# Optimization experiments

Hardware: AMD Instinct MI355X
Metric: run time of the kernel (lower is better)

Reference implementation:

```python
import jax, jax.numpy as jnp
import numpy as np

V, E, H, OUT = 32000, 256, 256, 32000
B, TE, TD = 16, 128, 64


def gru_layer(x, h0, Wih, Whh, bih, bhh, lengths):
    """PyTorch-semantics GRU over padded batch-first x:(B,T,I), h0:(B,H).
    Emulates pack/pad: hidden frozen and output zeroed past each sample's length."""
    T = x.shape[1]

    def step(h, inp):
        xt, t = inp  # xt:(B,I)
        gi = xt @ Wih.T + bih          # (B,3H)
        gh = h @ Whh.T + bhh
        ir, iz, inn = jnp.split(gi, 3, axis=-1)
        hr, hz, hn = jnp.split(gh, 3, axis=-1)
        r = jax.nn.sigmoid(ir + hr)
        z = jax.nn.sigmoid(iz + hz)
        n = jnp.tanh(inn + r * hn)
        hnew = (1.0 - z) * n + z * h
        valid = (t < lengths)[:, None]
        h = jnp.where(valid, hnew, h)
        out = jnp.where(valid, hnew, 0.0)
        return h, out

    hT, ys = jax.lax.scan(step, h0, (jnp.swapaxes(x, 0, 1), jnp.arange(T)))
    return jnp.swapaxes(ys, 0, 1), hT  # (B,T,H), (B,H)


def setup_inputs() -> dict:
    key = jax.random.key(0)
    ks = jax.random.split(key, 20)
    s = 0.05
    enc_len = jax.random.randint(ks[0], (B,), 1, TE + 1).at[0].set(TE)
    dec_len = jax.random.randint(ks[1], (B,), 1, TD + 1).at[0].set(TD)
    return {
        "encoder_input": jax.random.randint(ks[2], (B, TE), 0, V),
        "encoder_length": enc_len,
        "decoder_input": jax.random.randint(ks[3], (B, TD), 0, V),
        "decoder_length": dec_len,
        "embedding": jax.random.normal(ks[4], (V, E)) * s,
        "enc_Wih": jax.random.normal(ks[5], (3 * H, E)) * s,
        "enc_Whh": jax.random.normal(ks[6], (3 * H, H)) * s,
        "enc_bih": jax.random.normal(ks[7], (3 * H,)) * s,
        "enc_bhh": jax.random.normal(ks[8], (3 * H,)) * s,
        "dec_Wih": jax.random.normal(ks[9], (3 * H, E)) * s,
        "dec_Whh": jax.random.normal(ks[10], (3 * H, H)) * s,
        "dec_bih": jax.random.normal(ks[11], (3 * H,)) * s,
        "dec_bhh": jax.random.normal(ks[12], (3 * H,)) * s,
        "attn_W": jax.random.normal(ks[13], (H, 2 * H)) * s,
        "attn_Wb": jnp.zeros((H,)),
        "attn_v": jax.random.normal(ks[14], (1, H)) * s,
        "attn_vb": jnp.zeros((1,)),
        "dense_W": jax.random.normal(ks[15], (H, 2 * H)) * s,
        "dense_b": jnp.zeros((H,)),
        "out_W": jax.random.normal(ks[16], (OUT, H)) * s,
        "out_b": jnp.zeros((OUT,)),
    }


def reference(encoder_input, encoder_length, decoder_input, decoder_length,
              embedding, enc_Wih, enc_Whh, enc_bih, enc_bhh,
              dec_Wih, dec_Whh, dec_bih, dec_bhh,
              attn_W, attn_Wb, attn_v, attn_vb,
              dense_W, dense_b, out_W, out_b):
    enc_x = embedding[encoder_input]  # (B,TE,E)
    dec_x = embedding[decoder_input]  # (B,TD,E)

    h0 = jnp.zeros((B, H), dtype=enc_x.dtype)
    enc_out, enc_h = gru_layer(enc_x, h0, enc_Wih, enc_Whh, enc_bih, enc_bhh, encoder_length)
    dec_out, _ = gru_layer(dec_x, enc_h, dec_Wih, dec_Whh, dec_bih, dec_bhh, decoder_length)

    # --- additive attention with per-sample length mask ---
    enc_valid = jnp.arange(TE) < encoder_length[:, None]     # (B,TE)
    dec_valid = jnp.arange(TD) < decoder_length[:, None]     # (B,TD)
    mask = (dec_valid[:, :, None] & enc_valid[:, None, :]).astype(enc_out.dtype)[..., None]  # (B,TD,TE,1)

    enc_e = enc_out[:, None, :, :] * mask  # (B,TD,TE,H)
    dec_e = dec_out[:, :, None, :] * mask  # (B,TD,TE,H)

    score = jnp.tanh(jnp.concatenate([enc_e, dec_e], axis=3) @ attn_W.T + attn_Wb)
    energy = score @ attn_v.T + attn_vb  # (B,TD,TE,1)
    a = jax.nn.softmax(energy, axis=2)   # softmax over encoder steps (unmasked, as original)
    aw = a * mask
    s = aw.sum(axis=2)                   # (B,TD,1)
    s = jnp.where(s == 0, 1.0, s)
    attention = aw / s[:, :, None, :]
    context = (attention * enc_e).sum(axis=2)  # (B,TD,H); dropout is identity (eval)

    outputs = jnp.concatenate([dec_out, context], axis=2)  # (B,TD,2H)
    dense = jnp.tanh(outputs @ dense_W.T + dense_b)
    logits = dense @ out_W.T + out_b  # (B,TD,OUT)
    return logits
```

## Files before the change

### kernel.cpp

```cpp
#include <hip/hip_runtime.h>
#include <hip/hip_bf16.h>

typedef unsigned short ushort_t;
typedef unsigned int uint_t;
typedef unsigned long long u64_t;

#define BB 16
#define TE 128
#define TD 64
#define HH 256
#define G3 768
#define KK 256
#define OUTV 32000
#define MROWS_E (BB*TE)
#define MROWS_D (BB*TD)
#define NBLK 16
#define JD 16
#define QW_PER_BUF 2048

typedef __attribute__((ext_vector_type(8))) short short8;
typedef __attribute__((ext_vector_type(4))) float f32x4;

__device__ __forceinline__ float b2f(ushort_t u) {
  union { uint_t i; float f; } v; v.i = ((uint_t)u) << 16; return v.f;
}
__device__ __forceinline__ ushort_t f2b(float f) {
  union { float f; uint_t i; } v; v.f = f;
  uint_t x = v.i;
  return (ushort_t)((x + 0x7fffu + ((x >> 16) & 1u)) >> 16);
}
__device__ __forceinline__ float ldf(const void* p, size_t i, uint_t f32f) {
  return f32f ? ((const float*)p)[i] : b2f(((const ushort_t*)p)[i]);
}
__device__ __forceinline__ float fsig(float x) { return 1.f/(1.f + __expf(-x)); }
__device__ __forceinline__ float ftanh(float x) { return 1.f - 2.f/(__expf(2.f*x) + 1.f); }

__global__ __launch_bounds__(256) void detect_kernel(const void* emb, uint_t* flag) {
  int tid = threadIdx.x;
  uint_t w = ((const uint_t*)emb)[tid];
  uint_t e = (w >> 7) & 0xFFu;
  bool pass = (e >= 100u && e <= 127u);
  unsigned long long m = __ballot(pass);
  __shared__ int cnt[4];
  if ((tid & 63) == 0) cnt[tid >> 6] = __popcll(m);
  __syncthreads();
  if (tid == 0) {
    int c = cnt[0] + cnt[1] + cnt[2] + cnt[3];
    *flag = (c >= 128) ? 0u : 1u;
  }
}

__global__ __launch_bounds__(256) void prep_kernel(
    const void* eWhh, const void* dWhh, const void* denseW, const void* outW,
    const void* ebih, const void* ebhh, const void* dbih, const void* dbhh,
    const void* outb, const uint_t* flagp,
    ushort_t* WBe, ushort_t* WBd, ushort_t* DWT, ushort_t* obW,
    float* cbe, float* cbd, float* obf, u64_t* hq) {
  uint_t f = *flagp;
  int tid = blockIdx.x * blockDim.x + threadIdx.x;
  int nth = gridDim.x * blockDim.x;
  for (int i = tid; i < G3*KK; i += nth) {
    WBe[i] = f2b(ldf(eWhh, i, f));
    WBd[i] = f2b(ldf(dWhh, i, f));
  }
  for (int i = tid; i < 512*HH; i += nth) {
    int k = i / HH, c = i % HH;
    DWT[i] = f2b(ldf(denseW, (size_t)c*512 + k, f));
  }
  for (size_t i = tid; i < (size_t)OUTV*HH; i += nth) obW[i] = f2b(ldf(outW, i, f));
  for (int i = tid; i < G3; i += nth) {
    float be = ldf(ebih, i, f), bd = ldf(dbih, i, f);
    if (i < 2*HH) { be += ldf(ebhh, i, f); bd += ldf(dbhh, i, f); }
    cbe[i] = be; cbd[i] = bd;
  }
  for (int i = tid; i < OUTV; i += nth) obf[i] = ldf(outb, i, f);
  for (int i = tid; i < 2*QW_PER_BUF; i += nth) hq[i] = 0ull;
}

#define LDT 264

__global__ __launch_bounds__(256) void gemm_kernel(
    const ushort_t* A, const int* tokens, const void* emb,
    const void* Bw, int ldb, int b_off,
    const float* bias, const uint_t* flagp,
    float* Cf, ushort_t* Cb, int ldc, int M, int tshift, int a_f32, int b_bf16) {
  __shared__ __align__(16) ushort_t Bs[64*LDT];
  __shared__ __align__(16) ushort_t As[32*LDT];
  uint_t f = *flagp;
  int tid = threadIdx.x;
  int wave = tid >> 6, lane = tid & 63;
  int n0 = blockIdx.x * 64;
#pragma unroll
  for (int it = 0; it < 8; ++it) {
    int idx = it*256 + tid;
    int row = idx >> 5, col = (idx & 31) << 3;
    size_t e = (size_t)(n0 + row)*ldb + col + b_off;
    uint4 v;
    if (f && !b_bf16) {
      const float4* s = (const float4*)((const float*)Bw + e);
      float4 x = s[0], y = s[1];
      v.x = (uint_t)f2b(x.x) | ((uint_t)f2b(x.y) << 16);
      v.y = (uint_t)f2b(x.z) | ((uint_t)f2b(x.w) << 16);
      v.z = (uint_t)f2b(y.x) | ((uint_t)f2b(y.y) << 16);
      v.w = (uint_t)f2b(y.z) | ((uint_t)f2b(y.w) << 16);
    } else {
      v = *(const uint4*)((const ushort_t*)Bw + e);
    }
    *(uint4*)(Bs + row*LDT + col) = v;
  }
  int arow_i = lane & 15;
  float bias_v = 0.f;
  if (bias) bias_v = bias[n0 + wave*16 + arow_i];
  int koff = (lane >> 4) << 3;
  for (int m0 = blockIdx.y*32; m0 < M; m0 += gridDim.y*32) {
    __syncthreads();
#pragma unroll
    for (int it = 0; it < 4; ++it) {
      int idx = it*256 + tid;
      int row = idx >> 5, col = (idx & 31) << 3;
      uint4 v;
      if (tokens) {
        size_t e = (size_t)tokens[m0 + row]*KK + col;
        if (f) {
          const float4* s = (const float4*)((const float*)emb + e);
          float4 x = s[0], y = s[1];
          v.x = (uint_t)f2b(x.x) | ((uint_t)f2b(x.y) << 16);
          v.y = (uint_t)f2b(x.z) | ((uint_t)f2b(x.w) << 16);
          v.z = (uint_t)f2b(y.x) | ((uint_t)f2b(y.y) << 16);
          v.w = (uint_t)f2b(y.z) | ((uint_t)f2b(y.w) << 16);
        } else {
          v = *(const uint4*)((const ushort_t*)emb + e);
        }
      } else if (a_f32) {
        const float4* s = (const float4*)((const float*)A + (size_t)(m0 + row)*KK + col);
        float4 x = s[0], y = s[1];
        v.x = (uint_t)f2b(x.x) | ((uint_t)f2b(x.y) << 16);
        v.y = (uint_t)f2b(x.z) | ((uint_t)f2b(x.w) << 16);
        v.z = (uint_t)f2b(y.x) | ((uint_t)f2b(y.y) << 16);
        v.w = (uint_t)f2b(y.z) | ((uint_t)f2b(y.w) << 16);
      } else {
        v = *(const uint4*)(A + (size_t)(m0 + row)*KK + col);
      }
      *(uint4*)(As + row*LDT + col) = v;
    }
    __syncthreads();
#pragma unroll
    for (int msub = 0; msub < 2; ++msub) {
      f32x4 acc = {0.f,0.f,0.f,0.f};
      const ushort_t* ap = As + (msub*16 + arow_i)*LDT + koff;
      const ushort_t* bp = Bs + (wave*16 + arow_i)*LDT + koff;
#pragma unroll
      for (int ks = 0; ks < 8; ++ks) {
        short8 af = *(const short8*)(ap + ks*32);
        short8 bf = *(const short8*)(bp + ks*32);
        acc = __builtin_amdgcn_mfma_f32_16x16x32_bf16(af, bf, acc, 0, 0, 0);
      }
      int mbase = m0 + msub*16 + (lane >> 4)*4;
      int ncol = n0 + wave*16 + arow_i;
#pragma unroll
      for (int r = 0; r < 4; ++r) {
        float val = acc[r] + bias_v;
        int mr = mbase + r;
        int orow = tshift ? (((mr & ((1 << tshift) - 1)) << 4) + (mr >> tshift)) : mr;
        if (Cf) Cf[(size_t)orow*ldc + ncol] = val;
        else    Cb[(size_t)orow*ldc + ncol] = f2b(val);
      }
    }
  }
}

#define HSBF 264

__device__ __forceinline__ void stage_w(const ushort_t* WB, int j0, int tid,
                                        ushort_t* wlds) {
#pragma unroll
  for (int it = 0; it < 6; ++it) {
    int idx = it*256 + tid;
    int row = idx >> 5, col = (idx & 31) << 3;
    const ushort_t* src = WB + ((size_t)((row >> 4)*HH + j0 + (row & 15)))*KK + col;
    *(uint4*)(wlds + row*HSBF + col) = *(const uint4*)src;
  }
}

__global__ __launch_bounds__(256) void gru_kernel(
    const float* gi_e, const float* gi_d, const ushort_t* WBe, const ushort_t* WBd,
    const void* ebhh, const void* dbhh, const uint_t* flagp,
    const int* elen, const int* dlen, float* eout, float* dout, u64_t* hq) {
  uint_t f = *flagp;
  __shared__ __align__(16) ushort_t wlds[48*HSBF];
  __shared__ __align__(16) float part[2][4][3][16][17];
  const int tid = threadIdx.x;
  const int wave = tid >> 6, lane = tid & 63;
  const int mrow = lane & 15, quad = lane >> 4;
  const int j0 = blockIdx.x * JD;
  const int m = tid >> 4, n = tid & 15;
  const int j = j0 + n;
  const int je = j & ~1;
  const int widx = ((je >> 6) << 9) + (((je >> 5) & 1) << 8)
                 + (((je >> 1) & 3) << 6) + (((je >> 3) & 3) << 4) + m;

  stage_w(WBe, j0, tid, wlds);
  const float bn_e = ldf(ebhh, 2*HH + j, f);
  const float bn_d = ldf(dbhh, 2*HH + j, f);
  const int len_e = elen[m], len_d = dlen[m];
  float hreg = 0.f;
  float grv = gi_e[(size_t)m*G3 + j];
  float gzv = gi_e[(size_t)m*G3 + HH + j];
  float gnv = gi_e[(size_t)m*G3 + 2*HH + j];
  __syncthreads();

  for (int s = 0; s < TE + TD; ++s) {
    if (s == TE) {
      stage_w(WBd, j0, tid, wlds);
      __syncthreads();
    }
    const bool enc = s < TE;
    const int t = enc ? s : s - TE;
    const u64_t* hbR = hq + (size_t)(s & 1)*QW_PER_BUF + wave*512 + lane;
    u64_t qv[8];
    const uint_t target = (uint_t)s;
    int guard = 0;
    for (;;) {
      bool ok = true;
#pragma unroll
      for (int ks = 0; ks < 2; ++ks)
#pragma unroll
        for (int i = 0; i < 4; ++i) {
          qv[ks*4 + i] = __hip_atomic_load(hbR + ks*256 + i*64,
                                           __ATOMIC_RELAXED, __HIP_MEMORY_SCOPE_AGENT);
          ok = ok && ((uint_t)qv[ks*4 + i] == target);
        }
      if (__all(ok) || ++guard > 30000) break;
    }
    f32x4 ar = {0.f,0.f,0.f,0.f}, az = {0.f,0.f,0.f,0.f}, an = {0.f,0.f,0.f,0.f};
#pragma unroll
    for (int ks = 0; ks < 2; ++ks) {
      union { uint_t u[4]; short8 s8; } av;
#pragma unroll
      for (int i = 0; i < 4; ++i) av.u[i] = (uint_t)(qv[ks*4 + i] >> 32);
      const ushort_t* wp = wlds + mrow*HSBF + wave*64 + ks*32 + quad*8;
      short8 b0 = *(const short8*)(wp);
      short8 b1 = *(const short8*)(wp + 16*HSBF);
      short8 b2 = *(const short8*)(wp + 32*HSBF);
      ar = __builtin_amdgcn_mfma_f32_16x16x32_bf16(av.s8, b0, ar, 0, 0, 0);
      az = __builtin_amdgcn_mfma_f32_16x16x32_bf16(av.s8, b1, az, 0, 0, 0);
      an = __builtin_amdgcn_mfma_f32_16x16x32_bf16(av.s8, b2, an, 0, 0, 0);
    }
    const int p = s & 1;
#pragma unroll
    for (int r = 0; r < 4; ++r) {
      part[p][wave][0][quad*4 + r][mrow] = ar[r];
      part[p][wave][1][quad*4 + r][mrow] = az[r];
      part[p][wave][2][quad*4 + r][mrow] = an[r];
    }
    __syncthreads();
    float accr = 0.f, accz = 0.f, accn = 0.f;
#pragma unroll
    for (int w = 0; w < 4; ++w) {
      accr += part[p][w][0][m][n];
      accz += part[p][w][1][m][n];
      accn += part[p][w][2][m][n];
    }
    float rr = fsig(grv + accr);
    float zz = fsig(gzv + accz);
    float nn = ftanh(gnv + rr*(accn + (enc ? bn_e : bn_d)));
    float hc = (1.f - zz)*nn + zz*hreg;
    bool valid = t < (enc ? len_e : len_d);
    float ov = valid ? hc : 0.f;
    hreg = valid ? hc : hreg;
    if (enc) eout[((size_t)(m*TE + t))*HH + j] = ov;
    else     dout[((size_t)(m*TD + t))*HH + j] = ov;
    uint_t h16 = (uint_t)f2b(hreg);
    uint_t up = (uint_t)__shfl_down((int)h16, 1);
    if (!(n & 1)) {
      u64_t q = ((u64_t)(h16 | (up << 16)) << 32) | (u64_t)(uint_t)(s + 1);
      __hip_atomic_store(hq + (size_t)((s + 1) & 1)*QW_PER_BUF + widx,
                         q, __ATOMIC_RELAXED, __HIP_MEMORY_SCOPE_AGENT);
    }
    int s2 = s + 1;
    if (s2 < TE + TD) {
      const float* g2 = (s2 < TE) ? (gi_e + (size_t)(s2*BB + m)*G3)
                                  : (gi_d + (size_t)((s2 - TE)*BB + m)*G3);
      grv = g2[j]; gzv = g2[HH + j]; gnv = g2[2*HH + j];
    }
  }
}

__global__ __launch_bounds__(256) void attn_kernel(
    const float* eprj, const float* dprj, const float* eout, const float* dout,
    const void* Wb, const void* av, const void* avb,
    const ushort_t* DWT, const void* db, const uint_t* flagp,
    const int* elen, const int* dlen, ushort_t* dense_bf) {
  int bd = blockIdx.x;
  int b = bd / TD, td = bd % TD;
  int tid = threadIdx.x;
  int wave = tid >> 6, lane = tid & 63;
  uint_t f = *flagp;
  __shared__ float dp[HH], dsrow[HH], vv[HH], att[TE];
  int el = elen[b];
  bool dok = td < dlen[b];
  size_t drow = (size_t)bd * HH;
  dp[tid] = dprj[drow + tid] + ldf(Wb, tid, f);
  dsrow[tid] = dout[drow + tid];
  vv[tid] = ldf(av, tid, f);
  if (tid < TE) att[tid] = 0.f;
  __syncthreads();
  float ctx = 0.f;
  if (dok) {
    float vb0 = ldf(avb, 0, f);
    int nteb = (el + 3) >> 2;
    for (int teb = 0; teb < nteb; ++teb) {
      int te = teb*4 + wave;
      if (te < el) {
        const float* ep = eprj + (size_t)(b*TE + te)*HH;
        float s = 0.f;
#pragma unroll
        for (int i = 0; i < 4; ++i) {
          int hh = lane + 64*i;
          s += ftanh(ep[hh] + dp[hh]) * vv[hh];
        }
#pragma unroll
        for (int off = 32; off > 0; off >>= 1) s += __shfl_xor(s, off);
        if (lane == 0) att[te] = s + vb0;
      }
    }
    __syncthreads();
    float mx = -1e30f;
    for (int te = 0; te < el; ++te) mx = fmaxf(mx, att[te]);
    __syncthreads();
    if (tid < el) att[tid] = __expf(att[tid] - mx);
    __syncthreads();
    float ssum = 0.f;
    for (int te = 0; te < el; ++te) ssum += att[te];
    float inv = (ssum > 0.f) ? 1.f/ssum : 0.f;
    const float* ebase = eout + (size_t)(b*TE)*HH + tid;
    float c0 = 0.f, c1 = 0.f, c2 = 0.f, c3 = 0.f;
    int te = 0;
    for (; te + 4 <= el; te += 4) {
      c0 += att[te    ] * ebase[(size_t)(te    )*HH];
      c1 += att[te + 1] * ebase[(size_t)(te + 1)*HH];
      c2 += att[te + 2] * ebase[(size_t)(te + 2)*HH];
      c3 += att[te + 3] * ebase[(size_t)(te + 3)*HH];
    }
    for (; te < el; ++te) c0 += att[te] * ebase[(size_t)te*HH];
    ctx = (c0 + c1 + c2 + c3) * inv;
  }
  __syncthreads();
  dp[tid] = ctx;
  __syncthreads();
  const ushort_t* w0 = DWT + tid;
  float a0 = ldf(db, tid, f), a1 = 0.f, a2 = 0.f, a3 = 0.f;
#pragma unroll 8
  for (int k = 0; k < HH; k += 4) {
    a0 = fmaf(b2f(w0[(size_t)(k    )*HH]), dsrow[k    ], a0);
    a1 = fmaf(b2f(w0[(size_t)(k + 1)*HH]), dsrow[k + 1], a1);
    a2 = fmaf(b2f(w0[(size_t)(k + 2)*HH]), dsrow[k + 2], a2);
    a3 = fmaf(b2f(w0[(size_t)(k + 3)*HH]), dsrow[k + 3], a3);
  }
#pragma unroll 8
  for (int k = 0; k < HH; k += 4) {
    a0 = fmaf(b2f(w0[(size_t)(HH + k    )*HH]), dp[k    ], a0);
    a1 = fmaf(b2f(w0[(size_t)(HH + k + 1)*HH]), dp[k + 1], a1);
    a2 = fmaf(b2f(w0[(size_t)(HH + k + 2)*HH]), dp[k + 2], a2);
    a3 = fmaf(b2f(w0[(size_t)(HH + k + 3)*HH]), dp[k + 3], a3);
  }
  dense_bf[drow + tid] = f2b(ftanh(a0 + a1 + a2 + a3));
}

extern "C" void kernel_launch(void* const* d_in, const int* in_sizes, int n_in,
                              void* d_out, int out_size, void* d_ws, size_t ws_size,
                              hipStream_t stream) {
  const int* enc_in   = (const int*)d_in[0];
  const int* enc_len  = (const int*)d_in[1];
  const int* dec_in   = (const int*)d_in[2];
  const int* dec_len  = (const int*)d_in[3];
  const void* emb    = d_in[4];
  const void* eWih   = d_in[5];
  const void* eWhh   = d_in[6];
  const void* ebih   = d_in[7];
  const void* ebhh   = d_in[8];
  const void* dWih   = d_in[9];
  const void* dWhh   = d_in[10];
  const void* dbih   = d_in[11];
  const void* dbhh   = d_in[12];
  const void* attnW  = d_in[13];
  const void* attnWb = d_in[14];
  const void* attnv  = d_in[15];
  const void* attnvb = d_in[16];
  const void* denseW = d_in[17];
  const void* denseb = d_in[18];
  const void* outW   = d_in[19];
  const void* outb   = d_in[20];
  float* out = (float*)d_out;

  float* ws = (float*)d_ws;
  size_t o = 0;
  uint_t* flag = (uint_t*)(ws + o);   o += 4;
  u64_t* hq = (u64_t*)(ws + o);       o += 4*QW_PER_BUF;
  ushort_t* WBe = (ushort_t*)(ws + o); o += G3*KK/2;
  ushort_t* WBd = (ushort_t*)(ws + o); o += G3*KK/2;
  ushort_t* DWT = (ushort_t*)(ws + o); o += 512*HH/2;
  ushort_t* obW = (ushort_t*)(ws + o); o += (size_t)OUTV*HH/2;
  float* cbe = ws + o;                o += G3;
  float* cbd = ws + o;                o += G3;
  float* obf = ws + o;                o += OUTV;
  float* gi_e = ws + o;               o += (size_t)MROWS_E*G3;
  float* gi_d = ws + o;               o += (size_t)MROWS_D*G3;
  float* eout = ws + o;               o += (size_t)MROWS_E*HH;
  float* dout = ws + o;               o += (size_t)MROWS_D*HH;
  float* eprj = ws + o;               o += (size_t)MROWS_E*HH;
  float* dprj = ws + o;               o += (size_t)MROWS_D*HH;
  ushort_t* dense_bf = (ushort_t*)(ws + o); o += (size_t)MROWS_D*HH/2;

  detect_kernel<<<1, 256, 0, stream>>>(emb, flag);
  prep_kernel<<<384, 256, 0, stream>>>(eWhh, dWhh, denseW, outW, ebih, ebhh, dbih,
                                       dbhh, outb, flag, WBe, WBd, DWT, obW,
                                       cbe, cbd, obf, hq);
  gemm_kernel<<<dim3(12,8), 256, 0, stream>>>(nullptr, enc_in, emb, eWih, 256, 0,
                                              cbe, flag, gi_e, nullptr, G3, MROWS_E, 7, 0, 0);
  gemm_kernel<<<dim3(12,4), 256, 0, stream>>>(nullptr, dec_in, emb, dWih, 256, 0,
                                              cbd, flag, gi_d, nullptr, G3, MROWS_D, 6, 0, 0);
  gru_kernel<<<NBLK, 256, 0, stream>>>(gi_e, gi_d, WBe, WBd, ebhh, dbhh, flag,
                                       enc_len, dec_len, eout, dout, hq);
  gemm_kernel<<<dim3(4,16), 256, 0, stream>>>((const ushort_t*)eout, nullptr, nullptr,
                                              attnW, 512, 0, nullptr, flag, eprj,
                                              nullptr, HH, MROWS_E, 0, 1, 0);
  gemm_kernel<<<dim3(4,8), 256, 0, stream>>>((const ushort_t*)dout, nullptr, nullptr,
                                             attnW, 512, 256, nullptr, flag, dprj,
                                             nullptr, HH, MROWS_D, 0, 1, 0);
  attn_kernel<<<MROWS_D, 256, 0, stream>>>(eprj, dprj, eout, dout, attnWb, attnv, attnvb,
                                           DWT, denseb, flag, enc_len, dec_len, dense_bf);
  gemm_kernel<<<dim3(500,4), 256, 0, stream>>>(dense_bf, nullptr, nullptr, obW, 256, 0,
                                               obf, flag, out, nullptr, OUTV, MROWS_D, 0, 0, 1);
}
```

Baseline: 786.4 us.

## Use single-wave GRU blocks, fuse dtype detection into prep, vectorize outW conversion

The recurrent GRU kernel now runs one 64-lane wave per block, which does the full K=256 reduction with 8 MFMA steps. This removes the per-step LDS partial-sum exchange and __syncthreads, shortening the latency-bound serial chain of 192 steps. The cost is 4x more polled atomic loads per lane and longer MFMA chains in a single wave. Separately, the dtype-detect kernel is merged into prep_kernel, saving a launch, and the 32000x256 output weight conversion now moves 8 elements per iteration with vector loads and stores.

After: 936.8 us. 19.1% more time.

```diff
diff --git a/kernel.cpp b/kernel.cpp
--- a/kernel.cpp
+++ b/kernel.cpp
@@ -35,39 +35,48 @@
 __device__ __forceinline__ float fsig(float x) { return 1.f/(1.f + __expf(-x)); }
 __device__ __forceinline__ float ftanh(float x) { return 1.f - 2.f/(__expf(2.f*x) + 1.f); }
 
-__global__ __launch_bounds__(256) void detect_kernel(const void* emb, uint_t* flag) {
-  int tid = threadIdx.x;
-  uint_t w = ((const uint_t*)emb)[tid];
+__global__ __launch_bounds__(256) void prep_kernel(
+    const void* emb, const void* eWhh, const void* dWhh, const void* denseW,
+    const void* outW, const void* ebih, const void* ebhh, const void* dbih,
+    const void* dbhh, const void* outb, uint_t* flag,
+    ushort_t* WBe, ushort_t* WBd, ushort_t* DWT, ushort_t* obW,
+    float* cbe, float* cbd, float* obf, u64_t* hq) {
+  int ltid = threadIdx.x;
+  uint_t w = ((const uint_t*)emb)[ltid];
   uint_t e = (w >> 7) & 0xFFu;
   bool pass = (e >= 100u && e <= 127u);
-  unsigned long long m = __ballot(pass);
+  unsigned long long mb = __ballot(pass);
   __shared__ int cnt[4];
-  if ((tid & 63) == 0) cnt[tid >> 6] = __popcll(m);
+  if ((ltid & 63) == 0) cnt[ltid >> 6] = __popcll(mb);
   __syncthreads();
-  if (tid == 0) {
-    int c = cnt[0] + cnt[1] + cnt[2] + cnt[3];
-    *flag = (c >= 128) ? 0u : 1u;
-  }
-}
-
-__global__ __launch_bounds__(256) void prep_kernel(
-    const void* eWhh, const void* dWhh, const void* denseW, const void* outW,
-    const void* ebih, const void* ebhh, const void* dbih, const void* dbhh,
-    const void* outb, const uint_t* flagp,
-    ushort_t* WBe, ushort_t* WBd, ushort_t* DWT, ushort_t* obW,
-    float* cbe, float* cbd, float* obf, u64_t* hq) {
-  uint_t f = *flagp;
-  int tid = blockIdx.x * blockDim.x + threadIdx.x;
+  int c = cnt[0] + cnt[1] + cnt[2] + cnt[3];
+  uint_t f = (c >= 128) ? 0u : 1u;
+  if (blockIdx.x == 0 && ltid == 0) *flag = f;
+  int tid = blockIdx.x * blockDim.x + ltid;
   int nth = gridDim.x * blockDim.x;
   for (int i = tid; i < G3*KK; i += nth) {
     WBe[i] = f2b(ldf(eWhh, i, f));
     WBd[i] = f2b(ldf(dWhh, i, f));
   }
   for (int i = tid; i < 512*HH; i += nth) {
-    int k = i / HH, c = i % HH;
-    DWT[i] = f2b(ldf(denseW, (size_t)c*512 + k, f));
-  }
-  for (size_t i = tid; i < (size_t)OUTV*HH; i += nth) obW[i] = f2b(ldf(outW, i, f));
+    int k = i / HH, cc = i % HH;
+    DWT[i] = f2b(ldf(denseW, (size_t)cc*512 + k, f));
+  }
+  const int OW8 = OUTV*HH/8;
+  for (int i = tid; i < OW8; i += nth) {
+    uint4 v;
+    if (f) {
+      const float4* s = (const float4*)outW + (size_t)i*2;
+      float4 x = s[0], y = s[1];
+      v.x = (uint_t)f2b(x.x) | ((uint_t)f2b(x.y) << 16);
+      v.y = (uint_t)f2b(x.z) | ((uint_t)f2b(x.w) << 16);
+      v.z = (uint_t)f2b(y.x) | ((uint_t)f2b(y.y) << 16);
+      v.w = (uint_t)f2b(y.z) | ((uint_t)f2b(y.w) << 16);
+    } else {
+      v = ((const uint4*)outW)[i];
+    }
+    ((uint4*)obW)[i] = v;
+  }
   for (int i = tid; i < G3; i += nth) {
     float be = ldf(ebih, i, f), bd = ldf(dbih, i, f);
     if (i < 2*HH) { be += ldf(ebhh, i, f); bd += ldf(dbhh, i, f); }
@@ -171,74 +180,75 @@
 
 #define HSBF 264
 
-__device__ __forceinline__ void stage_w(const ushort_t* WB, int j0, int tid,
-                                        ushort_t* wlds) {
-#pragma unroll
-  for (int it = 0; it < 6; ++it) {
-    int idx = it*256 + tid;
+__device__ __forceinline__ void stage_w64(const ushort_t* WB, int j0, int lane,
+                                          ushort_t* wlds) {
+#pragma unroll
+  for (int it = 0; it < 24; ++it) {
+    int idx = it*64 + lane;
     int row = idx >> 5, col = (idx & 31) << 3;
     const ushort_t* src = WB + ((size_t)((row >> 4)*HH + j0 + (row & 15)))*KK + col;
     *(uint4*)(wlds + row*HSBF + col) = *(const uint4*)src;
   }
 }
 
-__global__ __launch_bounds__(256) void gru_kernel(
+__global__ __launch_bounds__(64, 1) void gru_kernel(
     const float* gi_e, const float* gi_d, const ushort_t* WBe, const ushort_t* WBd,
     const void* ebhh, const void* dbhh, const uint_t* flagp,
     const int* elen, const int* dlen, float* eout, float* dout, u64_t* hq) {
   uint_t f = *flagp;
   __shared__ __align__(16) ushort_t wlds[48*HSBF];
-  __shared__ __align__(16) float part[2][4][3][16][17];
-  const int tid = threadIdx.x;
-  const int wave = tid >> 6, lane = tid & 63;
-  const int mrow = lane & 15, quad = lane >> 4;
-  const int j0 = blockIdx.x * JD;
-  const int m = tid >> 4, n = tid & 15;
-  const int j = j0 + n;
-  const int je = j & ~1;
-  const int widx = ((je >> 6) << 9) + (((je >> 5) & 1) << 8)
-                 + (((je >> 1) & 3) << 6) + (((je >> 3) & 3) << 4) + m;
-
-  stage_w(WBe, j0, tid, wlds);
+  const int lane = threadIdx.x;
+  const int l15 = lane & 15, quad = lane >> 4;
+  const int wreg = blockIdx.x;
+  const int j0 = wreg * JD;
+  const int j = j0 + l15;
+
+  stage_w64(WBe, j0, lane, wlds);
   const float bn_e = ldf(ebhh, 2*HH + j, f);
   const float bn_d = ldf(dbhh, 2*HH + j, f);
-  const int len_e = elen[m], len_d = dlen[m];
-  float hreg = 0.f;
-  float grv = gi_e[(size_t)m*G3 + j];
-  float gzv = gi_e[(size_t)m*G3 + HH + j];
-  float gnv = gi_e[(size_t)m*G3 + 2*HH + j];
-  __syncthreads();
+  int lene_r[4], lend_r[4];
+#pragma unroll
+  for (int r = 0; r < 4; ++r) {
+    lene_r[r] = elen[quad*4 + r];
+    lend_r[r] = dlen[quad*4 + r];
+  }
+  float hreg[4] = {0.f, 0.f, 0.f, 0.f};
+  float gr[4], gz[4], gn[4];
+#pragma unroll
+  for (int r = 0; r < 4; ++r) {
+    const float* gp = gi_e + (size_t)(quad*4 + r)*G3;
+    gr[r] = gp[j]; gz[r] = gp[HH + j]; gn[r] = gp[2*HH + j];
+  }
+  const int pubbase = wreg*128 + (l15 >> 1)*16 + quad*4;
+  const bool dopub = !(l15 & 1);
 
   for (int s = 0; s < TE + TD; ++s) {
-    if (s == TE) {
-      stage_w(WBd, j0, tid, wlds);
-      __syncthreads();
-    }
+    if (s == TE) stage_w64(WBd, j0, lane, wlds);
     const bool enc = s < TE;
     const int t = enc ? s : s - TE;
-    const u64_t* hbR = hq + (size_t)(s & 1)*QW_PER_BUF + wave*512 + lane;
-    u64_t qv[8];
+    const u64_t* hbR = hq + (size_t)(s & 1)*QW_PER_BUF + quad*64 + l15;
+    u64_t qv[32];
     const uint_t target = (uint_t)s;
     int guard = 0;
     for (;;) {
       bool ok = true;
 #pragma unroll
-      for (int ks = 0; ks < 2; ++ks)
-#pragma unroll
-        for (int i = 0; i < 4; ++i) {
-          qv[ks*4 + i] = __hip_atomic_load(hbR + ks*256 + i*64,
+      for (int ks = 0; ks < 8; ++ks)
+#pragma unroll
+        for (int e = 0; e < 4; ++e) {
+          qv[ks*4 + e] = __hip_atomic_load(hbR + ks*256 + e*16,
                                            __ATOMIC_RELAXED, __HIP_MEMORY_SCOPE_AGENT);
-          ok = ok && ((uint_t)qv[ks*4 + i] == target);
+          ok = ok && ((uint_t)qv[ks*4 + e] == target);
         }
       if (__all(ok) || ++guard > 30000) break;
     }
     f32x4 ar = {0.f,0.f,0.f,0.f}, az = {0.f,0.f,0.f,0.f}, an = {0.f,0.f,0.f,0.f};
 #pragma unroll
-    for (int ks = 0; ks < 2; ++ks) {
+    for (int ks = 0; ks < 8; ++ks) {
       union { uint_t u[4]; short8 s8; } av;
 #pragma unroll
-      for (int i = 0; i < 4; ++i) av.u[i] = (uint_t)(qv[ks*4 + i] >> 32);
-      const ushort_t* wp = wlds + mrow*HSBF + wave*64 + ks*32 + quad*8;
+      for (int e = 0; e < 4; ++e) av.u[e] = (uint_t)(qv[ks*4 + e] >> 32);
+      const ushort_t* wp = wlds + l15*HSBF + ks*32 + quad*8;
       short8 b0 = *(const short8*)(wp);
       short8 b1 = *(const short8*)(wp + 16*HSBF);
       short8 b2 = *(const short8*)(wp + 32*HSBF);
@@ -246,42 +256,43 @@
       az = __builtin_amdgcn_mfma_f32_16x16x32_bf16(av.s8, b1, az, 0, 0, 0);
       an = __builtin_amdgcn_mfma_f32_16x16x32_bf16(av.s8, b2, an, 0, 0, 0);
     }
-    const int p = s & 1;
+    const float bn = enc ? bn_e : bn_d;
 #pragma unroll
     for (int r = 0; r < 4; ++r) {
-      part[p][wave][0][quad*4 + r][mrow] = ar[r];
-      part[p][wave][1][quad*4 + r][mrow] = az[r];
-      part[p][wave][2][quad*4 + r][mrow] = an[r];
-    }
-    __syncthreads();
-    float accr = 0.f, accz = 0.f, accn = 0.f;
-#pragma unroll
-    for (int w = 0; w < 4; ++w) {
-      accr += part[p][w][0][m][n];
-      accz += part[p][w][1][m][n];
-      accn += part[p][w][2][m][n];
-    }
-    float rr = fsig(grv + accr);
-    float zz = fsig(gzv + accz);
-    float nn = ftanh(gnv + rr*(accn + (enc ? bn_e : bn_d)));
-    float hc = (1.f - zz)*nn + zz*hreg;
-    bool valid = t < (enc ? len_e : len_d);
-    float ov = valid ? hc : 0.f;
-    hreg = valid ? hc : hreg;
-    if (enc) eout[((size_t)(m*TE + t))*HH + j] = ov;
-    else     dout[((size_t)(m*TD + t))*HH + j] = ov;
-    uint_t h16 = (uint_t)f2b(hreg);
-    uint_t up = (uint_t)__shfl_down((int)h16, 1);
-    if (!(n & 1)) {
-      u64_t q = ((u64_t)(h16 | (up << 16)) << 32) | (u64_t)(uint_t)(s + 1);
-      __hip_atomic_store(hq + (size_t)((s + 1) & 1)*QW_PER_BUF + widx,
-                         q, __ATOMIC_RELAXED, __HIP_MEMORY_SCOPE_AGENT);
+      float rr = fsig(gr[r] + ar[r]);
+      float zz = fsig(gz[r] + az[r]);
+      float nn = ftanh(gn[r] + rr*(an[r] + bn));
+      float hc = (1.f - zz)*nn + zz*hreg[r];
+      bool valid = t < (enc ? lene_r[r] : lend_r[r]);
+      float ov = valid ? hc : 0.f;
+      hreg[r] = valid ? hc : hreg[r];
+      int m = quad*4 + r;
+      if (enc) eout[((size_t)(m*TE + t))*HH + j] = ov;
+      else     dout[((size_t)(m*TD + t))*HH + j] = ov;
+    }
+    uint_t h16[4], up[4];
+#pragma unroll
+    for (int r = 0; r < 4; ++r) {
+      h16[r] = (uint_t)f2b(hreg[r]);
+      up[r] = (uint_t)__shfl_down((int)h16[r], 1);
+    }
+    if (dopub) {
+      u64_t* hbW = hq + (size_t)((s + 1) & 1)*QW_PER_BUF + pubbase;
+#pragma unroll
+      for (int r = 0; r < 4; ++r) {
+        u64_t q = ((u64_t)(h16[r] | (up[r] << 16)) << 32) | (u64_t)(uint_t)(s + 1);
+        __hip_atomic_store(hbW + r, q, __ATOMIC_RELAXED, __HIP_MEMORY_SCOPE_AGENT);
+      }
     }
     int s2 = s + 1;
     if (s2 < TE + TD) {
-      const float* g2 = (s2 < TE) ? (gi_e + (size_t)(s2*BB + m)*G3)
-                                  : (gi_d + (size_t)((s2 - TE)*BB + m)*G3);
-      grv = g2[j]; gzv = g2[HH + j]; gnv = g2[2*HH + j];
+      const float* gbase = (s2 < TE) ? gi_e + (size_t)(s2*BB)*G3
+                                     : gi_d + (size_t)((s2 - TE)*BB)*G3;
+#pragma unroll
+      for (int r = 0; r < 4; ++r) {
+        const float* gp = gbase + (size_t)(quad*4 + r)*G3;
+        gr[r] = gp[j]; gz[r] = gp[HH + j]; gn[r] = gp[2*HH + j];
+      }
     }
   }
 }
@@ -412,16 +423,15 @@
   float* dprj = ws + o;               o += (size_t)MROWS_D*HH;
   ushort_t* dense_bf = (ushort_t*)(ws + o); o += (size_t)MROWS_D*HH/2;
 
-  detect_kernel<<<1, 256, 0, stream>>>(emb, flag);
-  prep_kernel<<<384, 256, 0, stream>>>(eWhh, dWhh, denseW, outW, ebih, ebhh, dbih,
-                                       dbhh, outb, flag, WBe, WBd, DWT, obW,
+  prep_kernel<<<384, 256, 0, stream>>>(emb, eWhh, dWhh, denseW, outW, ebih, ebhh,
+                                       dbih, dbhh, outb, flag, WBe, WBd, DWT, obW,
                                        cbe, cbd, obf, hq);
   gemm_kernel<<<dim3(12,8), 256, 0, stream>>>(nullptr, enc_in, emb, eWih, 256, 0,
                                               cbe, flag, gi_e, nullptr, G3, MROWS_E, 7, 0, 0);
   gemm_kernel<<<dim3(12,4), 256, 0, stream>>>(nullptr, dec_in, emb, dWih, 256, 0,
                                               cbd, flag, gi_d, nullptr, G3, MROWS_D, 6, 0, 0);
-  gru_kernel<<<NBLK, 256, 0, stream>>>(gi_e, gi_d, WBe, WBd, ebhh, dbhh, flag,
-                                       enc_len, dec_len, eout, dout, hq);
+  gru_kernel<<<NBLK, 64, 0, stream>>>(gi_e, gi_d, WBe, WBd, ebhh, dbhh, flag,
+                                      enc_len, dec_len, eout, dout, hq);
   gemm_kernel<<<dim3(4,16), 256, 0, stream>>>((const ushort_t*)eout, nullptr, nullptr,
                                               attnW, 512, 0, nullptr, flag, eprj,
                                               nullptr, HH, MROWS_E, 0, 1, 0);
```
